# Kernel tuning notes

Hardware: AMD Instinct MI355X
Metric: run time of the kernel (lower is better)

Reference implementation:

```python
import jax, jax.numpy as jnp
import numpy as np

# Grid / problem constants (match init_kwargs: shape=[15,400,400], batch_size=2)
B, D, H, W = 2, 15, 400, 400
N = 200000          # active voxels
CIN, COUT = 32, 64
# 27 kernel offsets for ksize=3, dilation=1, centered (submanifold alignment)
OFFS = np.array([[dz, dy, dx]
                 for dz in (-1, 0, 1)
                 for dy in (-1, 0, 1)
                 for dx in (-1, 0, 1)], dtype=np.int32)  # [27, 3]


def setup_inputs() -> dict:
    rng = np.random.default_rng(0)
    # unique active voxel coordinates (sorted flat indices for locality)
    flat = np.sort(rng.choice(B * D * H * W, size=N, replace=False)).astype(np.int64)
    b = flat // (D * H * W)
    r = flat % (D * H * W)
    z = r // (H * W)
    r = r % (H * W)
    y = r // W
    x = r % W
    coors = jnp.asarray(np.stack([b, z, y, x], axis=1).astype(np.int32))  # [N,4]

    key = jax.random.key(0)
    k1, k2, k3 = jax.random.split(key, 3)
    features = jax.random.normal(k1, (N, CIN), jnp.float32)
    W1 = jax.random.normal(k2, (27, CIN, COUT), jnp.float32) * (1.0 / np.sqrt(27.0 * CIN))
    W2 = jax.random.normal(k3, (27, COUT, COUT), jnp.float32) * (1.0 / np.sqrt(27.0 * COUT))
    return {"features": features, "coors": coors, "batch_size": B, "W1": W1, "W2": W2}


def _neighbor_table(coors):
    """Rulebook: for each of 27 offsets, index of the neighboring active voxel (-1 if none)."""
    n = coors.shape[0]
    flat = ((coors[:, 0] * D + coors[:, 1]) * H + coors[:, 2]) * W + coors[:, 3]
    # dense voxel hash: flat coord -> row index, -1 = inactive
    table = jnp.full((B * D * H * W,), -1, jnp.int32).at[flat].set(
        jnp.arange(n, dtype=jnp.int32))
    offs = jnp.asarray(OFFS)  # [27,3]
    z = coors[None, :, 1] + offs[:, 0:1]  # [27,N]
    y = coors[None, :, 2] + offs[:, 1:2]
    x = coors[None, :, 3] + offs[:, 2:3]
    valid = (z >= 0) & (z < D) & (y >= 0) & (y < H) & (x >= 0) & (x < W)
    nflat = ((coors[None, :, 0] * D + jnp.clip(z, 0, D - 1)) * H
             + jnp.clip(y, 0, H - 1)) * W + jnp.clip(x, 0, W - 1)
    nbr = table[nflat]                      # [27, N]
    return jnp.where(valid, nbr, -1)


def _subm_conv(feats, nbr, Wk):
    """Gather-GEMM-scatter submanifold conv: out[i] = sum_k W[k] @ feats[nbr[k,i]]."""
    out = jnp.zeros((feats.shape[0], Wk.shape[-1]), feats.dtype)
    for k in range(nbr.shape[0]):  # fixed 27-iteration loop over kernel offsets
        j = nbr[k]
        valid = j >= 0
        g = jnp.where(valid[:, None], feats[jnp.where(valid, j, 0)], 0.0)  # [N,Cin]
        out = out + g @ Wk[k]
    return out


def reference(features, coors, batch_size, W1, W2):
    # Submanifold conv preserves the active set -> rulebook is shared by both layers.
    nbr = _neighbor_table(coors)
    x = _subm_conv(features, nbr, W1)   # [N, COUT]
    x = _subm_conv(x, nbr, W2)          # [N, COUT]
    return x
```

## Files before the change

### kernel.cpp

```cpp
#include <hip/hip_runtime.h>
#include <hip/hip_bf16.h>

#define DD 15
#define HH 400
#define WW 400
#define CIN 32
#define COUT 64
#define KK 27
#define NVOX (2 * DD * HH * WW)
#define NWORDS (NVOX / 64)
#define CAP 32768
#define CNT_STRIDE 64
#define OFFC_GRID 2048
#define PCAP 262144
#define SCAN_B 1024

typedef short bf16x8 __attribute__((ext_vector_type(8)));
typedef float f32x4  __attribute__((ext_vector_type(4)));

__device__ inline short f2bf(float f) {
    unsigned u = __float_as_uint(f);
    return (short)((u + 0x7FFFu + ((u >> 16) & 1u)) >> 16);
}
__device__ inline float bflo(unsigned u) { return __uint_as_float(u << 16); }
__device__ inline float bfhi(unsigned u) { return __uint_as_float(u & 0xFFFF0000u); }

__global__ void init_kernel(unsigned long long* __restrict__ bitmap,
                            int* __restrict__ cnt) {
    int t = blockIdx.x * blockDim.x + threadIdx.x;
    if (t < KK * CNT_STRIDE) cnt[t] = 0;
    int stride = gridDim.x * blockDim.x;
    for (int w = t; w < NWORDS; w += stride) bitmap[w] = 0ull;
}

__global__ void fill_kernel(const int* __restrict__ coors,
                            int* __restrict__ flats,
                            unsigned long long* __restrict__ bitmap, int n) {
    int i = blockIdx.x * blockDim.x + threadIdx.x;
    if (i >= n) return;
    int b = coors[i * 4 + 0];
    int z = coors[i * 4 + 1];
    int y = coors[i * 4 + 2];
    int x = coors[i * 4 + 3];
    int f = ((b * DD + z) * HH + y) * WW + x;
    flats[i] = f;
    atomicOr(&bitmap[f >> 6], 1ull << (f & 63));
}

__global__ void prefix_kernel(const int* __restrict__ flats,
                              int* __restrict__ prefix, int n) {
    int w = blockIdx.x * blockDim.x + threadIdx.x;
    if (w >= NWORDS) return;
    int target = w << 6;
    int lo = 0, hi = n;
    while (lo < hi) {
        int mid = (lo + hi) >> 1;
        if (flats[mid] < target) lo = mid + 1; else hi = mid;
    }
    prefix[w] = lo;
}

__device__ inline bool bm_test(const unsigned long long* __restrict__ bitmap, int f) {
    return (bitmap[f >> 6] >> (f & 63)) & 1ull;
}
__device__ inline int bm_rank(const unsigned long long* __restrict__ bitmap,
                              const int* __restrict__ prefix, int f) {
    int w = f >> 6, b = f & 63;
    unsigned long long m = bitmap[w];
    return prefix[w] + __popcll(m & ((1ull << b) - 1ull));
}

__global__ __launch_bounds__(256) void build_pairs_kernel(
        const int* __restrict__ flats,
        const unsigned long long* __restrict__ bitmap,
        const int* __restrict__ prefix,
        int* __restrict__ cnt, int* __restrict__ pairI,
        int* __restrict__ pairJ, int* __restrict__ percnt, int n) {
    __shared__ int lcnt[KK];
    __shared__ int lbase[KK];
    __shared__ int lpos[KK];
    int i = blockIdx.x * blockDim.x + threadIdx.x;
    if (threadIdx.x < KK) { lcnt[threadIdx.x] = 0; lpos[threadIdx.x] = 0; }
    __syncthreads();

    int f0 = 0, x = 0;
    unsigned vmask = 0;
    bool act = (i < n);
    if (act) {
        f0 = flats[i];
        x = f0 % WW;
        int rem = f0 / WW;
        int y = rem % HH;
        int z = (rem / HH) % DD;
#pragma unroll
        for (int p = 0; p < 9; ++p) {
            int dz = p / 3 - 1, dy = p % 3 - 1;
            int zn = z + dz, yn = y + dy;
            if (zn < 0 || zn >= DD || yn < 0 || yn >= HH) continue;
            int fn = f0 + dz * (HH * WW) + dy * WW;
            int kb = p * 3;
            if (x > 0 && bm_test(bitmap, fn - 1)) {
                vmask |= 1u << kb; atomicAdd(&lcnt[kb], 1);
            }
            if (kb + 1 != 13 && bm_test(bitmap, fn)) {
                vmask |= 1u << (kb + 1); atomicAdd(&lcnt[kb + 1], 1);
            }
            if (x < WW - 1 && bm_test(bitmap, fn + 1)) {
                vmask |= 1u << (kb + 2); atomicAdd(&lcnt[kb + 2], 1);
            }
        }
        percnt[i] = __popc(vmask);
    }
    __syncthreads();
    if (threadIdx.x < KK && lcnt[threadIdx.x] > 0)
        lbase[threadIdx.x] = atomicAdd(&cnt[threadIdx.x * CNT_STRIDE], lcnt[threadIdx.x]);
    __syncthreads();
    if (act && vmask) {
        int lt = 0;
#pragma unroll
        for (int p = 0; p < 9; ++p) {
            int kb = p * 3;
            if (!(vmask & (7u << kb))) continue;
            int dz = p / 3 - 1, dy = p % 3 - 1;
            int fn = f0 + dz * (HH * WW) + dy * WW;
#pragma unroll
            for (int d = 0; d < 3; ++d) {
                int k = kb + d;
                if (!(vmask & (1u << k))) continue;
                int j = bm_rank(bitmap, prefix, fn + d - 1);
                int pos = lbase[k] + atomicAdd(&lpos[k], 1);
                if (pos < CAP) {
                    pairI[k * CAP + pos] = (i << 5) | lt;
                    pairJ[k * CAP + pos] = j;
                }
                ++lt;
            }
        }
    }
}

__global__ void scan1pad_kernel(const int* __restrict__ pc, int* __restrict__ bsum,
                                const int* __restrict__ cnt, int* __restrict__ pairI,
                                int* __restrict__ pairJ, int n, int nscan) {
    __shared__ int red[256];
    if ((int)blockIdx.x >= nscan) {
        int k = blockIdx.x - nscan;
        int ck = min(cnt[k * CNT_STRIDE], CAP);
        int ckp = min((ck + 127) & ~127, CAP);
        for (int pos = ck + (int)threadIdx.x; pos < ckp; pos += blockDim.x) {
            pairI[k * CAP + pos] = (n << 5);
            pairJ[k * CAP + pos] = 0;
        }
        return;
    }
    int base = blockIdx.x * SCAN_B;
    int s = 0;
#pragma unroll
    for (int u = 0; u < 4; ++u) {
        int idx = base + u * 256 + threadIdx.x;
        if (idx < n) s += pc[idx];
    }
    red[threadIdx.x] = s; __syncthreads();
    for (int o = 128; o > 0; o >>= 1) {
        if ((int)threadIdx.x < o) red[threadIdx.x] += red[threadIdx.x + o];
        __syncthreads();
    }
    if (threadIdx.x == 0) bsum[blockIdx.x] = red[0];
}

__global__ void scan3_kernel(const int* __restrict__ pc, const int* __restrict__ bsum,
                             int* __restrict__ rowptr, int n, int nscan) {
    __shared__ int ts[256];
    __shared__ int bs[256];
    int v = ((int)threadIdx.x < nscan && (int)threadIdx.x < (int)blockIdx.x)
                ? bsum[threadIdx.x] : 0;
    bs[threadIdx.x] = v; __syncthreads();
    for (int o = 128; o > 0; o >>= 1) {
        if ((int)threadIdx.x < o) bs[threadIdx.x] += bs[threadIdx.x + o];
        __syncthreads();
    }
    int bbase = bs[0];

    int base = blockIdx.x * SCAN_B + threadIdx.x * 4;
    int e[4]; int s = 0;
#pragma unroll
    for (int u = 0; u < 4; ++u) {
        int idx = base + u;
        e[u] = (idx < n) ? pc[idx] : 0;
        s += e[u];
    }
    ts[threadIdx.x] = s; __syncthreads();
    for (int o = 1; o < 256; o <<= 1) {
        int t = ((int)threadIdx.x >= o) ? ts[threadIdx.x - o] : 0;
        __syncthreads();
        ts[threadIdx.x] += t;
        __syncthreads();
    }
    int run = ts[threadIdx.x] - s + bbase;
#pragma unroll
    for (int u = 0; u < 4; ++u) {
        int idx = base + u;
        if (idx < n) rowptr[idx] = run;
        run += e[u];
        if (idx == n - 1) rowptr[n] = run;
    }
}

template <int C, typename TIN, typename TOUT>
__global__ __launch_bounds__(256) void center_mfma_kernel(
        const TIN* __restrict__ xin, const float* __restrict__ Wc,
        const int* __restrict__ rowptr, const unsigned short* __restrict__ part,
        TOUT* __restrict__ xout, int n) {
    constexpr int KT = C / 32;
    int lane = threadIdx.x & 63;
    int mrow = lane & 15;
    int kgrp = lane >> 4;
    int wid = (blockIdx.x * blockDim.x + threadIdx.x) >> 6;
    int nwaves = (gridDim.x * blockDim.x) >> 6;

    bf16x8 bf[KT][4];
#pragma unroll
    for (int kt = 0; kt < KT; ++kt)
#pragma unroll
        for (int nt = 0; nt < 4; ++nt)
#pragma unroll
            for (int j = 0; j < 8; ++j)
                bf[kt][nt][j] = f2bf(Wc[(kt * 32 + kgrp * 8 + j) * 64 + nt * 16 + mrow]);

    int ntiles = (n + 15) >> 4;
    for (int t = wid; t < ntiles; t += nwaves) {
        int row = t * 16 + mrow;
        f32x4 zero = {0.f, 0.f, 0.f, 0.f};
        bf16x8 a[KT];
        if (row < n) {
            if constexpr (sizeof(TIN) == 4) {
                const float* xr = (const float*)xin + (size_t)row * C + kgrp * 8;
#pragma unroll
                for (int kt = 0; kt < KT; ++kt) {
                    float4 x0 = *(const float4*)(xr + kt * 32);
                    float4 x1 = *(const float4*)(xr + kt * 32 + 4);
                    a[kt][0] = f2bf(x0.x); a[kt][1] = f2bf(x0.y);
                    a[kt][2] = f2bf(x0.z); a[kt][3] = f2bf(x0.w);
                    a[kt][4] = f2bf(x1.x); a[kt][5] = f2bf(x1.y);
                    a[kt][6] = f2bf(x1.z); a[kt][7] = f2bf(x1.w);
                }
            } else {
                const unsigned short* xr = (const unsigned short*)xin + (size_t)row * C + kgrp * 8;
#pragma unroll
                for (int kt = 0; kt < KT; ++kt)
                    a[kt] = *(const bf16x8*)(xr + kt * 32);
            }
        } else {
#pragma unroll
            for (int kt = 0; kt < KT; ++kt)
#pragma unroll
                for (int j = 0; j < 8; ++j) a[kt][j] = 0;
        }
        f32x4 acc[4];
#pragma unroll
        for (int nt = 0; nt < 4; ++nt) {
            acc[nt] = zero;
#pragma unroll
            for (int kt = 0; kt < KT; ++kt)
                acc[nt] = __builtin_amdgcn_mfma_f32_16x16x32_bf16(a[kt], bf[kt][nt], acc[nt], 0, 0, 0);
        }
#pragma unroll
        for (int r = 0; r < 4; ++r) {
            int orow = t * 16 + kgrp * 4 + r;
            if (orow < n) {
                int s0 = rowptr[orow], s1 = rowptr[orow + 1];
                for (int s = s0; s < s1; ++s) {
                    uint2 q = *(const uint2*)(part + (size_t)s * 64 + mrow * 4);
                    acc[0][r] += bflo(q.x);
                    acc[1][r] += bfhi(q.x);
                    acc[2][r] += bflo(q.y);
                    acc[3][r] += bfhi(q.y);
                }
                if constexpr (sizeof(TOUT) == 4) {
#pragma unroll
                    for (int nt = 0; nt < 4; ++nt)
                        ((float*)xout)[(size_t)orow * 64 + nt * 16 + mrow] = acc[nt][r];
                } else {
#pragma unroll
                    for (int nt = 0; nt < 4; ++nt)
                        ((unsigned short*)xout)[(size_t)orow * 64 + nt * 16 + mrow] =
                            (unsigned short)f2bf(acc[nt][r]);
                }
            }
        }
    }
}

template <int C, typename TIN>
__global__ __launch_bounds__(256) void offc_mfma_kernel(
        const TIN* __restrict__ xin, const float* __restrict__ Wsrc,
        const int* __restrict__ cnt, const int* __restrict__ pairI,
        const int* __restrict__ pairJ, const int* __restrict__ rowptr,
        unsigned short* __restrict__ part, int n) {
    constexpr int KT = C / 32;
    __shared__ int pfx[KK + 1];
    int lane = threadIdx.x & 63;
    int wid = threadIdx.x >> 6;
    int mrow = lane & 15;
    int kgrp = lane >> 4;
    if (threadIdx.x == 0) {
        int acc = 0; pfx[0] = 0;
        for (int k = 0; k < KK; ++k) {
            int ck = min(cnt[k * CNT_STRIDE], CAP);
            acc += (ck + 127) >> 7;
            pfx[k + 1] = acc;
        }
    }
    __syncthreads();
    int T = pfx[KK];
    for (int g = blockIdx.x; g < T; g += gridDim.x) {
        int k = 0;
        while (pfx[k + 1] <= g) ++k;
        int chunk = g - pfx[k];
        const float* Wk = Wsrc + (size_t)k * C * 64;
        bf16x8 bf[KT][4];
#pragma unroll
        for (int kt = 0; kt < KT; ++kt)
#pragma unroll
            for (int nt = 0; nt < 4; ++nt)
#pragma unroll
                for (int j = 0; j < 8; ++j)
                    bf[kt][nt][j] = f2bf(Wk[(kt * 32 + kgrp * 8 + j) * 64 + nt * 16 + mrow]);
        int base = k * CAP + chunk * 128 + wid * 32;
#pragma unroll
        for (int half = 0; half < 2; ++half) {
            int b16 = base + half * 16;
            int jrow = pairJ[b16 + mrow];
            bf16x8 a[KT];
            if constexpr (sizeof(TIN) == 4) {
                const float* xr = (const float*)xin + (size_t)jrow * C + kgrp * 8;
#pragma unroll
                for (int kt = 0; kt < KT; ++kt) {
                    float4 x0 = *(const float4*)(xr + kt * 32);
                    float4 x1 = *(const float4*)(xr + kt * 32 + 4);
                    a[kt][0] = f2bf(x0.x); a[kt][1] = f2bf(x0.y);
                    a[kt][2] = f2bf(x0.z); a[kt][3] = f2bf(x0.w);
                    a[kt][4] = f2bf(x1.x); a[kt][5] = f2bf(x1.y);
                    a[kt][6] = f2bf(x1.z); a[kt][7] = f2bf(x1.w);
                }
            } else {
                const unsigned short* xr = (const unsigned short*)xin + (size_t)jrow * C + kgrp * 8;
#pragma unroll
                for (int kt = 0; kt < KT; ++kt)
                    a[kt] = *(const bf16x8*)(xr + kt * 32);
            }
            f32x4 zero = {0.f, 0.f, 0.f, 0.f};
            f32x4 acc[4];
#pragma unroll
            for (int nt = 0; nt < 4; ++nt) {
                acc[nt] = zero;
#pragma unroll
                for (int kt = 0; kt < KT; ++kt)
                    acc[nt] = __builtin_amdgcn_mfma_f32_16x16x32_bf16(a[kt], bf[kt][nt], acc[nt], 0, 0, 0);
            }
#pragma unroll
            for (int r = 0; r < 4; ++r) {
                int pk = pairI[b16 + kgrp * 4 + r];
                int ir = pk >> 5;
                if (ir < n) {
                    int dst = rowptr[ir] + (pk & 31);
                    if (dst < PCAP) {
                        uint2 q;
                        q.x = (unsigned)(unsigned short)f2bf(acc[0][r]) |
                              ((unsigned)(unsigned short)f2bf(acc[1][r]) << 16);
                        q.y = (unsigned)(unsigned short)f2bf(acc[2][r]) |
                              ((unsigned)(unsigned short)f2bf(acc[3][r]) << 16);
                        *(uint2*)(part + (size_t)dst * 64 + mrow * 4) = q;
                    }
                }
            }
        }
    }
}

extern "C" void kernel_launch(void* const* d_in, const int* in_sizes, int n_in,
                              void* d_out, int out_size, void* d_ws, size_t ws_size,
                              hipStream_t stream) {
    const float* feats = (const float*)d_in[0];
    const int*   coors = (const int*)d_in[1];
    const float* W1 = (const float*)d_in[3];
    const float* W2 = (const float*)d_in[4];
    float* out = (float*)d_out;

    int n = in_sizes[0] / CIN;

    char* ws = (char*)d_ws;
    size_t off = 0;
    unsigned short* x1 = (unsigned short*)(ws + off);
    off += ((size_t)n * COUT * 2 + 255) & ~(size_t)255;
    unsigned long long* bitmap = (unsigned long long*)(ws + off);
    off += ((size_t)NWORDS * 8 + 255) & ~(size_t)255;
    int* prefix = (int*)(ws + off);
    off += ((size_t)NWORDS * 4 + 255) & ~(size_t)255;
    int* flats = (int*)(ws + off);
    off += ((size_t)n * 4 + 255) & ~(size_t)255;
    int* percnt = (int*)(ws + off);
    off += ((size_t)n * 4 + 255) & ~(size_t)255;
    int* rowptr = (int*)(ws + off);
    off += ((size_t)(n + 1) * 4 + 255) & ~(size_t)255;
    int* bsum = (int*)(ws + off);
    off += (256 * 4 + 255) & ~(size_t)255;
    int* cnt = (int*)(ws + off);
    off += ((size_t)KK * CNT_STRIDE * 4 + 255) & ~(size_t)255;
    int* pairI = (int*)(ws + off);
    off += ((size_t)KK * CAP * 4 + 4096 + 255) & ~(size_t)255;
    int* pairJ = (int*)(ws + off);
    off += ((size_t)KK * CAP * 4 + 4096 + 255) & ~(size_t)255;
    unsigned short* part = (unsigned short*)(ws + off);

    int nscan = (n + SCAN_B - 1) / SCAN_B;
    int ntiles = (n + 15) / 16;
    int cgrid = (ntiles + 3) / 4;

    init_kernel<<<(NWORDS + 255) / 256, 256, 0, stream>>>(bitmap, cnt);
    fill_kernel<<<(n + 255) / 256, 256, 0, stream>>>(coors, flats, bitmap, n);
    prefix_kernel<<<(NWORDS + 255) / 256, 256, 0, stream>>>(flats, prefix, n);
    build_pairs_kernel<<<(n + 255) / 256, 256, 0, stream>>>(
        flats, bitmap, prefix, cnt, pairI, pairJ, percnt, n);
    scan1pad_kernel<<<nscan + KK, 256, 0, stream>>>(percnt, bsum, cnt, pairI, pairJ, n, nscan);
    scan3_kernel<<<nscan, 256, 0, stream>>>(percnt, bsum, rowptr, n, nscan);
    offc_mfma_kernel<CIN, float><<<OFFC_GRID, 256, 0, stream>>>(
        feats, W1, cnt, pairI, pairJ, rowptr, part, n);
    center_mfma_kernel<CIN, float, unsigned short><<<cgrid, 256, 0, stream>>>(
        feats, W1 + (size_t)13 * CIN * COUT, rowptr, part, x1, n);
    offc_mfma_kernel<COUT, unsigned short><<<OFFC_GRID, 256, 0, stream>>>(
        x1, W2, cnt, pairI, pairJ, rowptr, part, n);
    center_mfma_kernel<COUT, unsigned short, float><<<cgrid, 256, 0, stream>>>(
        x1, W2 + (size_t)13 * COUT * COUT, rowptr, part, out, n);
}
```

Measured before the change: 150.6 us.

## Fuse scan partials and pair padding into build_pairs, interleave pair arrays

Per-block percnt sums are now reduced inside build_pairs_kernel, and the last block to finish (found via an atomic ticket) pads the pair lists. This removes the scan1pad kernel launch. pairI/pairJ are merged into one int2 array, so the offc kernel loads each pair with a single load and shuffles the I indices across lanes instead of reloading them. The center kernel now processes two tiles per wave iteration with a halved grid. The last-block pattern relies on atomic visibility of cnt, and a block padding while others write is avoided only through the ticket ordering.

Result: no change. 153.1 us (+1.7%).

```diff
diff --git a/kernel.cpp b/kernel.cpp
--- a/kernel.cpp
+++ b/kernel.cpp
@@ -26,9 +26,10 @@
 __device__ inline float bfhi(unsigned u) { return __uint_as_float(u & 0xFFFF0000u); }
 
 __global__ void init_kernel(unsigned long long* __restrict__ bitmap,
-                            int* __restrict__ cnt) {
+                            int* __restrict__ cnt, int* __restrict__ done) {
     int t = blockIdx.x * blockDim.x + threadIdx.x;
     if (t < KK * CNT_STRIDE) cnt[t] = 0;
+    if (blockIdx.x == 0 && threadIdx.x == 0) *done = 0;
     int stride = gridDim.x * blockDim.x;
     for (int w = t; w < NWORDS; w += stride) bitmap[w] = 0ull;
 }
@@ -74,11 +75,15 @@
         const int* __restrict__ flats,
         const unsigned long long* __restrict__ bitmap,
         const int* __restrict__ prefix,
-        int* __restrict__ cnt, int* __restrict__ pairI,
-        int* __restrict__ pairJ, int* __restrict__ percnt, int n) {
+        int* __restrict__ cnt, int2* __restrict__ pairIJ,
+        int* __restrict__ percnt, int* __restrict__ bsum256,
+        int* __restrict__ done, int n) {
     __shared__ int lcnt[KK];
     __shared__ int lbase[KK];
     __shared__ int lpos[KK];
+    __shared__ int red[256];
+    __shared__ int lticket;
+    __shared__ int cks[KK];
     int i = blockIdx.x * blockDim.x + threadIdx.x;
     if (threadIdx.x < KK) { lcnt[threadIdx.x] = 0; lpos[threadIdx.x] = 0; }
     __syncthreads();
@@ -111,9 +116,15 @@
         }
         percnt[i] = __popc(vmask);
     }
+    red[threadIdx.x] = act ? (int)__popc(vmask) : 0;
     __syncthreads();
     if (threadIdx.x < KK && lcnt[threadIdx.x] > 0)
         lbase[threadIdx.x] = atomicAdd(&cnt[threadIdx.x * CNT_STRIDE], lcnt[threadIdx.x]);
+    for (int o = 128; o > 0; o >>= 1) {
+        if ((int)threadIdx.x < o) red[threadIdx.x] += red[threadIdx.x + o];
+        __syncthreads();
+    }
+    if (threadIdx.x == 0) bsum256[blockIdx.x] = red[0];
     __syncthreads();
     if (act && vmask) {
         int lt = 0;
@@ -129,51 +140,34 @@
                 if (!(vmask & (1u << k))) continue;
                 int j = bm_rank(bitmap, prefix, fn + d - 1);
                 int pos = lbase[k] + atomicAdd(&lpos[k], 1);
-                if (pos < CAP) {
-                    pairI[k * CAP + pos] = (i << 5) | lt;
-                    pairJ[k * CAP + pos] = j;
-                }
+                if (pos < CAP) pairIJ[k * CAP + pos] = make_int2((i << 5) | lt, j);
                 ++lt;
             }
         }
     }
-}
-
-__global__ void scan1pad_kernel(const int* __restrict__ pc, int* __restrict__ bsum,
-                                const int* __restrict__ cnt, int* __restrict__ pairI,
-                                int* __restrict__ pairJ, int n, int nscan) {
-    __shared__ int red[256];
-    if ((int)blockIdx.x >= nscan) {
-        int k = blockIdx.x - nscan;
-        int ck = min(cnt[k * CNT_STRIDE], CAP);
-        int ckp = min((ck + 127) & ~127, CAP);
-        for (int pos = ck + (int)threadIdx.x; pos < ckp; pos += blockDim.x) {
-            pairI[k * CAP + pos] = (n << 5);
-            pairJ[k * CAP + pos] = 0;
-        }
-        return;
-    }
-    int base = blockIdx.x * SCAN_B;
-    int s = 0;
-#pragma unroll
-    for (int u = 0; u < 4; ++u) {
-        int idx = base + u * 256 + threadIdx.x;
-        if (idx < n) s += pc[idx];
-    }
-    red[threadIdx.x] = s; __syncthreads();
-    for (int o = 128; o > 0; o >>= 1) {
-        if ((int)threadIdx.x < o) red[threadIdx.x] += red[threadIdx.x + o];
+    __syncthreads();
+    if (threadIdx.x == 0) lticket = atomicAdd(done, 1);
+    __syncthreads();
+    if (lticket == (int)gridDim.x - 1) {
+        if (threadIdx.x < KK)
+            cks[threadIdx.x] = atomicAdd(&cnt[threadIdx.x * CNT_STRIDE], 0);
         __syncthreads();
-    }
-    if (threadIdx.x == 0) bsum[blockIdx.x] = red[0];
-}
-
-__global__ void scan3_kernel(const int* __restrict__ pc, const int* __restrict__ bsum,
-                             int* __restrict__ rowptr, int n, int nscan) {
+        for (int k = 0; k < KK; ++k) {
+            int ck = min(cks[k], CAP);
+            int ckp = min((ck + 127) & ~127, CAP);
+            for (int pos = ck + (int)threadIdx.x; pos < ckp; pos += 256)
+                pairIJ[k * CAP + pos] = make_int2(n << 5, 0);
+        }
+    }
+}
+
+__global__ void scan3_kernel(const int* __restrict__ pc, const int* __restrict__ bsum256,
+                             int* __restrict__ rowptr, int n) {
     __shared__ int ts[256];
     __shared__ int bs[256];
-    int v = ((int)threadIdx.x < nscan && (int)threadIdx.x < (int)blockIdx.x)
-                ? bsum[threadIdx.x] : 0;
+    int lim = 4 * blockIdx.x;
+    int v = 0;
+    for (int j = threadIdx.x; j < lim; j += 256) v += bsum256[j];
     bs[threadIdx.x] = v; __syncthreads();
     for (int o = 128; o > 0; o >>= 1) {
         if ((int)threadIdx.x < o) bs[threadIdx.x] += bs[threadIdx.x + o];
@@ -228,7 +222,10 @@
                 bf[kt][nt][j] = f2bf(Wc[(kt * 32 + kgrp * 8 + j) * 64 + nt * 16 + mrow]);
 
     int ntiles = (n + 15) >> 4;
-    for (int t = wid; t < ntiles; t += nwaves) {
+    int ntiles2 = (ntiles + 1) >> 1;
+
+    auto body = [&](int t) {
+        if (t >= ntiles) return;
         int row = t * 16 + mrow;
         f32x4 zero = {0.f, 0.f, 0.f, 0.f};
         bf16x8 a[KT];
@@ -288,14 +285,19 @@
                 }
             }
         }
+    };
+
+    for (int tt = wid; tt < ntiles2; tt += nwaves) {
+        body(tt * 2);
+        body(tt * 2 + 1);
     }
 }
 
 template <int C, typename TIN>
 __global__ __launch_bounds__(256) void offc_mfma_kernel(
         const TIN* __restrict__ xin, const float* __restrict__ Wsrc,
-        const int* __restrict__ cnt, const int* __restrict__ pairI,
-        const int* __restrict__ pairJ, const int* __restrict__ rowptr,
+        const int* __restrict__ cnt, const int2* __restrict__ pairIJ,
+        const int* __restrict__ rowptr,
         unsigned short* __restrict__ part, int n) {
     constexpr int KT = C / 32;
     __shared__ int pfx[KK + 1];
@@ -330,7 +332,8 @@
 #pragma unroll
         for (int half = 0; half < 2; ++half) {
             int b16 = base + half * 16;
-            int jrow = pairJ[b16 + mrow];
+            int2 pA = pairIJ[b16 + mrow];
+            int jrow = pA.y;
             bf16x8 a[KT];
             if constexpr (sizeof(TIN) == 4) {
                 const float* xr = (const float*)xin + (size_t)jrow * C + kgrp * 8;
@@ -360,7 +363,7 @@
             }
 #pragma unroll
             for (int r = 0; r < 4; ++r) {
-                int pk = pairI[b16 + kgrp * 4 + r];
+                int pk = __shfl(pA.x, kgrp * 4 + r);
                 int ir = pk >> 5;
                 if (ir < n) {
                     int dst = rowptr[ir] + (pk & 31);
@@ -403,33 +406,34 @@
     off += ((size_t)n * 4 + 255) & ~(size_t)255;
     int* rowptr = (int*)(ws + off);
     off += ((size_t)(n + 1) * 4 + 255) & ~(size_t)255;
-    int* bsum = (int*)(ws + off);
-    off += (256 * 4 + 255) & ~(size_t)255;
+    int* bsum256 = (int*)(ws + off);
+    off += (1024 * 4 + 255) & ~(size_t)255;
+    int* done = (int*)(ws + off);
+    off += 256;
     int* cnt = (int*)(ws + off);
     off += ((size_t)KK * CNT_STRIDE * 4 + 255) & ~(size_t)255;
-    int* pairI = (int*)(ws + off);
-    off += ((size_t)KK * CAP * 4 + 4096 + 255) & ~(size_t)255;
-    int* pairJ = (int*)(ws + off);
-    off += ((size_t)KK * CAP * 4 + 4096 + 255) & ~(size_t)255;
+    int2* pairIJ = (int2*)(ws + off);
+    off += ((size_t)KK * CAP * 8 + 4096 + 255) & ~(size_t)255;
     unsigned short* part = (unsigned short*)(ws + off);
 
+    int nbuild = (n + 255) / 256;
     int nscan = (n + SCAN_B - 1) / SCAN_B;
     int ntiles = (n + 15) / 16;
-    int cgrid = (ntiles + 3) / 4;
-
-    init_kernel<<<(NWORDS + 255) / 256, 256, 0, stream>>>(bitmap, cnt);
+    int ntiles2 = (ntiles + 1) / 2;
+    int cgrid = (ntiles2 + 3) / 4;
+
+    init_kernel<<<(NWORDS + 255) / 256, 256, 0, stream>>>(bitmap, cnt, done);
     fill_kernel<<<(n + 255) / 256, 256, 0, stream>>>(coors, flats, bitmap, n);
     prefix_kernel<<<(NWORDS + 255) / 256, 256, 0, stream>>>(flats, prefix, n);
-    build_pairs_kernel<<<(n + 255) / 256, 256, 0, stream>>>(
-        flats, bitmap, prefix, cnt, pairI, pairJ, percnt, n);
-    scan1pad_kernel<<<nscan + KK, 256, 0, stream>>>(percnt, bsum, cnt, pairI, pairJ, n, nscan);
-    scan3_kernel<<<nscan, 256, 0, stream>>>(percnt, bsum, rowptr, n, nscan);
+    build_pairs_kernel<<<nbuild, 256, 0, stream>>>(
+        flats, bitmap, prefix, cnt, pairIJ, percnt, bsum256, done, n);
+    scan3_kernel<<<nscan, 256, 0, stream>>>(percnt, bsum256, rowptr, n);
     offc_mfma_kernel<CIN, float><<<OFFC_GRID, 256, 0, stream>>>(
-        feats, W1, cnt, pairI, pairJ, rowptr, part, n);
+        feats, W1, cnt, pairIJ, rowptr, part, n);
     center_mfma_kernel<CIN, float, unsigned short><<<cgrid, 256, 0, stream>>>(
         feats, W1 + (size_t)13 * CIN * COUT, rowptr, part, x1, n);
     offc_mfma_kernel<COUT, unsigned short><<<OFFC_GRID, 256, 0, stream>>>(
-        x1, W2, cnt, pairI, pairJ, rowptr, part, n);
+        x1, W2, cnt, pairIJ, rowptr, part, n);
     center_mfma_kernel<COUT, unsigned short, float><<<cgrid, 256, 0, stream>>>(
         x1, W2 + (size_t)13 * COUT * COUT, rowptr, part, out, n);
 }
```
